# Kernel tuning notes

Measured on AMD Instinct MI355X. Metric: run time of the kernel, lower is better.

The kernel has to match this reference:

```python
import jax, jax.numpy as jnp
import numpy as np

N_USERS = 50000
N_ENTITIES = 100000
N_FACTORS = 8
N_RELATIONS = 17  # weight has n_relations-1 = 16 rows
EMB = 64
N_EDGES = 2_000_000
NNZ = 2_000_000
SLOPE = 0.2


def setup_inputs() -> dict:
    key = jax.random.key(0)
    ks = jax.random.split(key, 16)
    inp = {
        "entity_emb": jax.random.normal(ks[0], (N_ENTITIES, EMB), jnp.float32),
        "user_emb": jax.random.normal(ks[1], (N_USERS, EMB), jnp.float32),
        "latent_emb": jax.random.normal(ks[2], (N_FACTORS, EMB), jnp.float32),
        "edge_index": jax.random.randint(ks[3], (2, N_EDGES), 0, N_ENTITIES, jnp.int32),
        "edge_type": jax.random.randint(ks[4], (N_EDGES,), 1, N_RELATIONS, jnp.int32),
        "interact_rows": jax.random.randint(ks[5], (NNZ,), 0, N_USERS, jnp.int32),
        "interact_cols": jax.random.randint(ks[6], (NNZ,), 0, N_ENTITIES, jnp.int32),
        "interact_vals": jax.random.uniform(ks[7], (NNZ,), jnp.float32),
        "weight": jax.random.normal(ks[8], (N_RELATIONS - 1, EMB), jnp.float32),
        "entity_cate_set": jax.random.randint(ks[9], (N_ENTITIES,), 1, 33, jnp.int32),
        # params (torch Linear convention: y = x @ W.T + b)
        "W_user_att": jax.random.normal(ks[10], (N_FACTORS, N_FACTORS), jnp.float32) * 0.1,
        "b_user_att": jnp.zeros((N_FACTORS,), jnp.float32),
        "W_weight_att": jax.random.normal(ks[11], (N_RELATIONS - 1, N_RELATIONS - 1), jnp.float32) * 0.1,
        "b_weight_att": jnp.zeros((N_RELATIONS - 1,), jnp.float32),
        "W1": jax.random.normal(ks[12], (EMB, EMB), jnp.float32) * 0.1,
        "b1": jnp.zeros((EMB,), jnp.float32),
        "W2": jax.random.normal(ks[13], (EMB, EMB), jnp.float32) * 0.1,
        "b2": jnp.zeros((EMB,), jnp.float32),
    }
    return inp


def _lin(x, W, b):
    return x @ W.T + b


def reference(entity_emb, user_emb, latent_emb, edge_index, edge_type,
              interact_rows, interact_cols, interact_vals, weight, entity_cate_set,
              W_user_att, b_user_att, W_weight_att, b_weight_att, W1, b1, W2, b2):
    head, tail = edge_index[0], edge_index[1]

    # KG aggregate: gather-multiply-scatter_mean (is_div=False branch)
    neigh = entity_emb[tail] * weight[edge_type - 1]            # [E, C]
    sums = jax.ops.segment_sum(neigh, head, num_segments=N_ENTITIES)
    cnt = jax.ops.segment_sum(jnp.ones((neigh.shape[0],), neigh.dtype),
                              head, num_segments=N_ENTITIES)
    entity_agg = sums / jnp.maximum(cnt, 1.0)[:, None]          # [N_ent, C]

    # user aggregate: sparse mm (COO) interact_mat @ entity_emb
    user_agg = jax.ops.segment_sum(interact_vals[:, None] * entity_emb[interact_cols],
                                   interact_rows, num_segments=N_USERS)  # [U, C]

    # user -> latent interest attention
    score_ = _lin(user_emb, W1, b1) @ _lin(latent_emb, W1, b1).T          # [U, F]
    score = jax.nn.softmax(jax.nn.leaky_relu(_lin(score_, W_user_att, b_user_att), SLOPE), axis=1)  # [U, F]

    score_rp = _lin(latent_emb, W2, b2) @ _lin(weight, W2, b2).T          # [F, R-1]
    latent_new = jax.nn.softmax(jax.nn.leaky_relu(_lin(score_rp, W_weight_att, b_weight_att), SLOPE), axis=-1) @ weight  # [F, C]

    # (disen_weight * score).sum(dim=1) == score @ latent_new
    user_agg = user_agg * (score @ latent_new) + user_agg
    return (entity_agg, user_agg, latent_new)
```

## Files before the change

### kernel.cpp

```cpp
#include <hip/hip_runtime.h>

#define N_USERS    50000
#define N_ENTITIES 100000
#define EMB        64
#define N_EDGES    2000000
#define NNZ        2000000
#define SLOPE      0.2f

#define KROWS   256
#define KSHIFT  8
#define NBK     391
#define UROWS   128
#define USHIFT  7
#define NBU     391
#define CAPK    8192
#define CAPU    7680
#define CHUNK   8192
#define EPT     (CHUNK / 512)
#define PB      ((N_EDGES + CHUNK - 1) / CHUNK)
#define NQ      (NBK + NBU)
#define ACCBLK  512

__global__ __launch_bounds__(512) void hist_both(const int* __restrict__ head,
                                                 const int* __restrict__ urows,
                                                 int* __restrict__ kgOffs,
                                                 int* __restrict__ uOffs) {
    __shared__ int lhk[NBK];
    __shared__ int lhu[NBU];
    int tid = threadIdx.x;
    for (int t = tid; t < NBK; t += 512) lhk[t] = 0;
    for (int t = tid; t < NBU; t += 512) lhu[t] = 0;
    __syncthreads();
    int base = blockIdx.x * CHUNK;
#pragma unroll 4
    for (int j = 0; j < EPT; ++j) {
        int i = base + j * 512 + tid;
        if (i < N_EDGES) atomicAdd(&lhk[head[i] >> KSHIFT], 1);
        if (i < NNZ)     atomicAdd(&lhu[urows[i] >> USHIFT], 1);
    }
    __syncthreads();
    for (int t = tid; t < NBK; t += 512) { int c = lhk[t]; if (c) atomicAdd(&kgOffs[t], c); }
    for (int t = tid; t < NBU; t += 512) { int c = lhu[t]; if (c) atomicAdd(&uOffs[t], c); }
}

__global__ __launch_bounds__(512) void scan_both(int* __restrict__ kgOffs,
                                                 int* __restrict__ kgCur,
                                                 int* __restrict__ uOffs,
                                                 int* __restrict__ uCur) {
    __shared__ int tsum[512];
    int n     = (blockIdx.x == 0) ? NBK : NBU;
    int* offs = (blockIdx.x == 0) ? kgOffs : uOffs;
    int* cur  = (blockIdx.x == 0) ? kgCur  : uCur;
    int tid = threadIdx.x;
    int v = (tid < n) ? offs[tid] : 0;
    tsum[tid] = v;
    __syncthreads();
    for (int off = 1; off < 512; off <<= 1) {
        int t = (tid >= off) ? tsum[tid - off] : 0;
        __syncthreads();
        tsum[tid] += t;
        __syncthreads();
    }
    if (tid < n) { int e = tsum[tid] - v; offs[tid] = e; cur[tid] = e; }
    if (tid == n - 1) offs[n] = tsum[tid];
}

__device__ void small_dense_body(int l,
                                 const float* __restrict__ latent_emb,
                                 const float* __restrict__ weight,
                                 const float* __restrict__ W_weight_att,
                                 const float* __restrict__ b_weight_att,
                                 const float* __restrict__ W1,
                                 const float* __restrict__ b1,
                                 const float* __restrict__ W2,
                                 const float* __restrict__ b2,
                                 float* __restrict__ P_out,
                                 float* __restrict__ c_out,
                                 float* __restrict__ latent_new_out) {
    __shared__ float lat1[8 * 64];
    __shared__ float lat2[8 * 64];
    __shared__ float wl2[16 * 64];
    __shared__ float srp[8 * 16];
    __shared__ float soft[8 * 16];

    if (l < 64) {
        for (int f = 0; f < 8; ++f) {
            float a1 = b1[l], a2 = b2[l];
            for (int k = 0; k < 64; ++k) {
                float le = latent_emb[f * 64 + k];
                a1 += le * W1[l * 64 + k];
                a2 += le * W2[l * 64 + k];
            }
            lat1[f * 64 + l] = a1;
            lat2[f * 64 + l] = a2;
        }
        for (int r = 0; r < 16; ++r) {
            float a = b2[l];
            for (int k = 0; k < 64; ++k) a += weight[r * 64 + k] * W2[l * 64 + k];
            wl2[r * 64 + l] = a;
        }
    }
    __syncthreads();

    if (l < 64) {
        for (int f = 0; f < 8; ++f) {
            float p = 0.f;
            for (int d = 0; d < 64; ++d) p += W1[d * 64 + l] * lat1[f * 64 + d];
            P_out[l * 8 + f] = p;
        }
        if (l < 8) {
            float cc = 0.f;
            for (int d = 0; d < 64; ++d) cc += b1[d] * lat1[l * 64 + d];
            c_out[l] = cc;
        }
        for (int idx = l; idx < 128; idx += 64) {
            int f = idx >> 4, r = idx & 15;
            float a = 0.f;
            for (int d = 0; d < 64; ++d) a += lat2[f * 64 + d] * wl2[r * 64 + d];
            srp[idx] = a;
        }
    }
    __syncthreads();

    if (l < 8) {
        int f = l;
        float att[16];
        float mx = -1e30f;
        for (int k = 0; k < 16; ++k) {
            float a = b_weight_att[k];
            for (int j = 0; j < 16; ++j) a += srp[f * 16 + j] * W_weight_att[k * 16 + j];
            a = a > 0.f ? a : SLOPE * a;
            att[k] = a;
            mx = fmaxf(mx, a);
        }
        float s = 0.f;
        for (int k = 0; k < 16; ++k) { att[k] = expf(att[k] - mx); s += att[k]; }
        float inv = 1.f / s;
        for (int k = 0; k < 16; ++k) soft[f * 16 + k] = att[k] * inv;
    }
    __syncthreads();

    if (l < 64) {
        for (int f = 0; f < 8; ++f) {
            float a = 0.f;
            for (int r = 0; r < 16; ++r) a += soft[f * 16 + r] * weight[r * 64 + l];
            latent_new_out[f * 64 + l] = a;
        }
    }
}

__global__ void small_dense(const float* __restrict__ latent_emb,
                            const float* __restrict__ weight,
                            const float* __restrict__ W_weight_att,
                            const float* __restrict__ b_weight_att,
                            const float* __restrict__ W1,
                            const float* __restrict__ b1,
                            const float* __restrict__ W2,
                            const float* __restrict__ b2,
                            float* __restrict__ P_out,
                            float* __restrict__ c_out,
                            float* __restrict__ latent_new_out) {
    small_dense_body(threadIdx.x, latent_emb, weight, W_weight_att, b_weight_att,
                     W1, b1, W2, b2, P_out, c_out, latent_new_out);
}

__global__ __launch_bounds__(512) void scatter_both(const int* __restrict__ head,
                                                    const int* __restrict__ tail,
                                                    const int* __restrict__ etype,
                                                    int* __restrict__ kgCur,
                                                    int* __restrict__ kgPay,
                                                    const int* __restrict__ urows,
                                                    const int* __restrict__ ucols,
                                                    const float* __restrict__ uvals,
                                                    int* __restrict__ uCur,
                                                    int2* __restrict__ uPay,
                                                    const float* __restrict__ latent_emb,
                                                    const float* __restrict__ weight,
                                                    const float* __restrict__ W_weight_att,
                                                    const float* __restrict__ b_weight_att,
                                                    const float* __restrict__ W1,
                                                    const float* __restrict__ b1,
                                                    const float* __restrict__ W2,
                                                    const float* __restrict__ b2,
                                                    float* __restrict__ Pbuf,
                                                    float* __restrict__ cbuf,
                                                    float* __restrict__ lat_out) {
    if (blockIdx.x == 2 * PB) {
        small_dense_body(threadIdx.x, latent_emb, weight, W_weight_att,
                         b_weight_att, W1, b1, W2, b2, Pbuf, cbuf, lat_out);
        return;
    }

    __shared__ int lh[NBK];
    __shared__ int lb[NBK];
    int tid = threadIdx.x;
    bool isKg = blockIdx.x < PB;
    int base = (isKg ? blockIdx.x : blockIdx.x - PB) * CHUNK;
    int nTot = isKg ? N_EDGES : NNZ;
    int shift = isKg ? KSHIFT : USHIFT;
    const int* src = isKg ? head : urows;
    int* cur = isKg ? kgCur : uCur;

    for (int t = tid; t < NBK; t += 512) lh[t] = 0;
    __syncthreads();

    int hreg[EPT];
#pragma unroll
    for (int j = 0; j < EPT; ++j) {
        int i = base + j * 512 + tid;
        int h = (i < nTot) ? src[i] : -1;
        hreg[j] = h;
        if (h >= 0) atomicAdd(&lh[h >> shift], 1);
    }
    __syncthreads();
    for (int t = tid; t < NBK; t += 512) {
        int c = lh[t];
        lb[t] = c ? atomicAdd(&cur[t], c) : 0;
        lh[t] = 0;
    }
    __syncthreads();
    if (isKg) {
#pragma unroll
        for (int j = 0; j < EPT; ++j) {
            int h = hreg[j];
            if (h >= 0) {
                int i = base + j * 512 + tid;
                int b = h >> KSHIFT;
                int p = lb[b] + atomicAdd(&lh[b], 1);
                kgPay[p] = tail[i] | ((etype[i] - 1) << 17) | ((h & (KROWS - 1)) << 21);
            }
        }
    } else {
#pragma unroll
        for (int j = 0; j < EPT; ++j) {
            int h = hreg[j];
            if (h >= 0) {
                int i = base + j * 512 + tid;
                int b = h >> USHIFT;
                int p = lb[b] + atomicAdd(&lh[b], 1);
                uPay[p] = make_int2(ucols[i] | ((h & (UROWS - 1)) << 17),
                                    __float_as_int(uvals[i]));
            }
        }
    }
}

__global__ __launch_bounds__(1024, 8) void acc_both(
        const int* __restrict__ kgPay, const int* __restrict__ kgOffs,
        const int2* __restrict__ uPay, const int* __restrict__ uOffs,
        const float* __restrict__ entity_emb,
        const float* __restrict__ weight,
        const float* __restrict__ user_emb,
        const float* __restrict__ P,
        const float* __restrict__ cvec,
        const float* __restrict__ W_user_att,
        const float* __restrict__ b_user_att,
        const float* __restrict__ latent_new,
        int* __restrict__ qCtr,
        float* __restrict__ ent_out,
        float* __restrict__ user_out) {
    __shared__ long long smem8[7873];
    __shared__ int sbk;
    int t = threadIdx.x, d = t & 63, wv = t >> 6;

    for (;;) {
        __syncthreads();
        if (t == 0) sbk = atomicAdd(qCtr, 1);
        __syncthreads();
        int q = sbk;
        if (q >= NQ) return;

        if (q < NBU) {
            int2* spay = (int2*)smem8;
            int* lcnt = (int*)(spay + CAPU);
            int* lofs = lcnt + UROWS;
            int* sc   = lofs + UROWS + 1;
            int bk = q;
            int start = uOffs[bk], end = uOffs[bk + 1];
            int n = end - start; if (n > CAPU) n = CAPU;

            if (t < UROWS) lcnt[t] = 0;
            __syncthreads();
            for (int i = t; i < n; i += 1024)
                atomicAdd(&lcnt[(uPay[start + i].x >> 17) & (UROWS - 1)], 1);
            __syncthreads();
            if (t < UROWS) sc[t] = lcnt[t];
            __syncthreads();
            for (int off = 1; off < UROWS; off <<= 1) {
                int v = (t < UROWS && t >= off) ? sc[t - off] : 0;
                __syncthreads();
                if (t < UROWS) sc[t] += v;
                __syncthreads();
            }
            if (t < UROWS) { int e = sc[t] - lcnt[t]; lofs[t] = e; lcnt[t] = e; }
            if (t == 0) lofs[UROWS] = n;
            __syncthreads();
            for (int i = t; i < n; i += 1024) {
                int2 v = uPay[start + i];
                int p = atomicAdd(&lcnt[(v.x >> 17) & (UROWS - 1)], 1);
                spay[p] = v;
            }
            __syncthreads();

            int rowbase = bk * UROWS;
            for (int rr = 0; rr < UROWS / 16; ++rr) {
                int r = wv * (UROWS / 16) + rr;
                int gr = rowbase + r;
                if (gr >= N_USERS) break;
                int s0 = lofs[r], e0 = lofs[r + 1];
                float acc = 0.f;
                int i = s0;
                for (; i + 7 < e0; i += 8) {
                    float a0 = 0.f, a1 = 0.f;
#pragma unroll
                    for (int u = 0; u < 8; u += 2) {
                        int2 va = spay[i + u], vb = spay[i + u + 1];
                        a0 += __int_as_float(va.y) * entity_emb[(va.x & 0x1FFFF) * EMB + d];
                        a1 += __int_as_float(vb.y) * entity_emb[(vb.x & 0x1FFFF) * EMB + d];
                    }
                    acc += a0 + a1;
                }
                for (; i < e0; ++i) {
                    int2 v = spay[i];
                    acc += __int_as_float(v.y) * entity_emb[(v.x & 0x1FFFF) * EMB + d];
                }
                for (int j = start + CAPU; j < end; ++j) {
                    int2 v = uPay[j];
                    if (((v.x >> 17) & (UROWS - 1)) == r)
                        acc += __int_as_float(v.y) * entity_emb[(v.x & 0x1FFFF) * EMB + d];
                }

                float ue = user_emb[gr * EMB + d];
                float s[8];
#pragma unroll
                for (int f = 0; f < 8; ++f) s[f] = ue * P[d * 8 + f];
#pragma unroll
                for (int off = 32; off; off >>= 1) {
#pragma unroll
                    for (int f = 0; f < 8; ++f) s[f] += __shfl_xor(s[f], off, 64);
                }
#pragma unroll
                for (int f = 0; f < 8; ++f) s[f] += cvec[f];
                float att[8];
                float mx = -1e30f;
#pragma unroll
                for (int k = 0; k < 8; ++k) {
                    float a = b_user_att[k];
#pragma unroll
                    for (int j = 0; j < 8; ++j) a += s[j] * W_user_att[k * 8 + j];
                    a = a > 0.f ? a : SLOPE * a;
                    att[k] = a;
                    mx = fmaxf(mx, a);
                }
                float sum = 0.f;
#pragma unroll
                for (int k = 0; k < 8; ++k) { att[k] = __expf(att[k] - mx); sum += att[k]; }
                float inv = 1.f / sum;
                float g = 0.f;
#pragma unroll
                for (int f = 0; f < 8; ++f) g += att[f] * inv * latent_new[f * EMB + d];
                user_out[gr * EMB + d] = acc * (1.f + g);
            }
        } else {
            int* spay = (int*)smem8;
            int* lcnt = spay + CAPK;
            int* lofs = lcnt + KROWS;
            int* sc   = lofs + KROWS + 1;
            int bk = q - NBU;
            int start = kgOffs[bk], end = kgOffs[bk + 1];
            int n = end - start; if (n > CAPK) n = CAPK;

            if (t < KROWS) lcnt[t] = 0;
            __syncthreads();
            for (int i = t; i < n; i += 1024)
                atomicAdd(&lcnt[(kgPay[start + i] >> 21) & (KROWS - 1)], 1);
            __syncthreads();
            if (t < KROWS) sc[t] = lcnt[t];
            __syncthreads();
            for (int off = 1; off < KROWS; off <<= 1) {
                int v = (t < KROWS && t >= off) ? sc[t - off] : 0;
                __syncthreads();
                if (t < KROWS) sc[t] += v;
                __syncthreads();
            }
            if (t < KROWS) { int e = sc[t] - lcnt[t]; lofs[t] = e; lcnt[t] = e; }
            if (t == 0) lofs[KROWS] = n;
            __syncthreads();
            for (int i = t; i < n; i += 1024) {
                int v = kgPay[start + i];
                int p = atomicAdd(&lcnt[(v >> 21) & (KROWS - 1)], 1);
                spay[p] = v;
            }
            __syncthreads();

            int rowbase = bk * KROWS;
            for (int rr = 0; rr < KROWS / 16; ++rr) {
                int r = wv * (KROWS / 16) + rr;
                int gr = rowbase + r;
                if (gr >= N_ENTITIES) break;
                int s0 = lofs[r], e0 = lofs[r + 1];
                int cnt = e0 - s0;
                float acc = 0.f;
                int i = s0;
                for (; i + 7 < e0; i += 8) {
                    float a0 = 0.f, a1 = 0.f;
#pragma unroll
                    for (int u = 0; u < 8; u += 2) {
                        int va = spay[i + u], vb = spay[i + u + 1];
                        a0 += entity_emb[(va & 0x1FFFF) * EMB + d] * weight[((va >> 17) & 15) * EMB + d];
                        a1 += entity_emb[(vb & 0x1FFFF) * EMB + d] * weight[((vb >> 17) & 15) * EMB + d];
                    }
                    acc += a0 + a1;
                }
                for (; i < e0; ++i) {
                    int v = spay[i];
                    acc += entity_emb[(v & 0x1FFFF) * EMB + d] * weight[((v >> 17) & 15) * EMB + d];
                }
                for (int j = start + CAPK; j < end; ++j) {
                    int v = kgPay[j];
                    if (((v >> 21) & (KROWS - 1)) == r) {
                        acc += entity_emb[(v & 0x1FFFF) * EMB + d] * weight[((v >> 17) & 15) * EMB + d];
                        ++cnt;
                    }
                }
                ent_out[gr * EMB + d] = acc / fmaxf((float)cnt, 1.f);
            }
        }
    }
}

__global__ void kg_scatter(const int* __restrict__ head, const int* __restrict__ tail,
                           const int* __restrict__ etype,
                           const float* __restrict__ entity_emb,
                           const float* __restrict__ weight,
                           float* __restrict__ sums, float* __restrict__ cnt) {
    int gid = blockIdx.x * blockDim.x + threadIdx.x;
    int e = gid >> 6, d = threadIdx.x & 63;
    if (e >= N_EDGES) return;
    int h = head[e], t = tail[e], w = etype[e] - 1;
    float v = entity_emb[t * EMB + d] * weight[w * EMB + d];
    unsafeAtomicAdd(&sums[h * EMB + d], v);
    if (d == 0) unsafeAtomicAdd(&cnt[h], 1.0f);
}

__global__ void user_scatter(const int* __restrict__ rows, const int* __restrict__ cols,
                             const float* __restrict__ vals,
                             const float* __restrict__ entity_emb,
                             float* __restrict__ user_sums) {
    int gid = blockIdx.x * blockDim.x + threadIdx.x;
    int e = gid >> 6, d = threadIdx.x & 63;
    if (e >= NNZ) return;
    float v = vals[e] * entity_emb[cols[e] * EMB + d];
    unsafeAtomicAdd(&user_sums[rows[e] * EMB + d], v);
}

__global__ void entity_div(float* __restrict__ ent, const float* __restrict__ cnt) {
    int gid = blockIdx.x * blockDim.x + threadIdx.x;
    if (gid >= N_ENTITIES * EMB) return;
    float c = cnt[gid >> 6];
    ent[gid] = ent[gid] / fmaxf(c, 1.0f);
}

__global__ void user_finalize(const float* __restrict__ user_emb,
                              const float* __restrict__ P,
                              const float* __restrict__ c,
                              const float* __restrict__ W_user_att,
                              const float* __restrict__ b_user_att,
                              const float* __restrict__ latent_new,
                              float* __restrict__ user_out) {
    int gid = blockIdx.x * blockDim.x + threadIdx.x;
    int u = gid >> 6, lane = threadIdx.x & 63;
    if (u >= N_USERS) return;
    float ue = user_emb[u * 64 + lane];
    float s[8];
#pragma unroll
    for (int f = 0; f < 8; ++f) s[f] = ue * P[lane * 8 + f];
#pragma unroll
    for (int off = 32; off; off >>= 1)
#pragma unroll
        for (int f = 0; f < 8; ++f) s[f] += __shfl_xor(s[f], off, 64);
#pragma unroll
    for (int f = 0; f < 8; ++f) s[f] += c[f];
    float att[8], mx = -1e30f;
#pragma unroll
    for (int k = 0; k < 8; ++k) {
        float a = b_user_att[k];
#pragma unroll
        for (int j = 0; j < 8; ++j) a += s[j] * W_user_att[k * 8 + j];
        a = a > 0.f ? a : SLOPE * a;
        att[k] = a;
        mx = fmaxf(mx, a);
    }
    float sum = 0.f;
#pragma unroll
    for (int k = 0; k < 8; ++k) { att[k] = expf(att[k] - mx); sum += att[k]; }
    float inv = 1.f / sum, g = 0.f;
#pragma unroll
    for (int f = 0; f < 8; ++f) g += att[f] * inv * latent_new[f * 64 + lane];
    float ua = user_out[u * 64 + lane];
    user_out[u * 64 + lane] = ua * (1.f + g);
}

extern "C" void kernel_launch(void* const* d_in, const int* in_sizes, int n_in,
                              void* d_out, int out_size, void* d_ws, size_t ws_size,
                              hipStream_t stream) {
    const float* entity_emb   = (const float*)d_in[0];
    const float* user_emb     = (const float*)d_in[1];
    const float* latent_emb   = (const float*)d_in[2];
    const int*   edge_index   = (const int*)d_in[3];
    const int*   edge_type    = (const int*)d_in[4];
    const int*   irows        = (const int*)d_in[5];
    const int*   icols        = (const int*)d_in[6];
    const float* ivals        = (const float*)d_in[7];
    const float* weight       = (const float*)d_in[8];
    const float* W_user_att   = (const float*)d_in[10];
    const float* b_user_att   = (const float*)d_in[11];
    const float* W_weight_att = (const float*)d_in[12];
    const float* b_weight_att = (const float*)d_in[13];
    const float* W1           = (const float*)d_in[14];
    const float* b1           = (const float*)d_in[15];
    const float* W2           = (const float*)d_in[16];
    const float* b2           = (const float*)d_in[17];

    float* out      = (float*)d_out;
    float* ent_out  = out;
    float* user_out = out + (size_t)N_ENTITIES * EMB;
    float* lat_out  = user_out + (size_t)N_USERS * EMB;

    const int* head = edge_index;
    const int* tail = edge_index + N_EDGES;

    int* ws_i = (int*)d_ws;
    int*   kgOffs = ws_i;
    int*   uOffs  = kgOffs + (NBK + 1);
    int*   qCtr   = uOffs + (NBU + 1);
    int*   kgCur  = qCtr + 2;
    int*   uCur   = kgCur + NBK;
    int*   kgPay  = uCur + NBU;
    int2*  uPay   = (int2*)(kgPay + N_EDGES);
    float* Pbuf   = (float*)(uPay + NNZ);
    float* cbuf   = Pbuf + 64 * 8;
    size_t need_bytes = (size_t)((NBK + 1) + (NBU + 1) + 2 + NBK + NBU +
                                 N_EDGES + 2 * (size_t)NNZ + 512 + 8) * 4;

    if (ws_size >= need_bytes) {
        hipMemsetAsync(kgOffs, 0,
                       (size_t)((NBK + 1) + (NBU + 1) + 2) * sizeof(int), stream);

        hist_both<<<PB, 512, 0, stream>>>(head, irows, kgOffs, uOffs);
        scan_both<<<2, 512, 0, stream>>>(kgOffs, kgCur, uOffs, uCur);
        scatter_both<<<2 * PB + 1, 512, 0, stream>>>(head, tail, edge_type, kgCur, kgPay,
                                                     irows, icols, ivals, uCur, uPay,
                                                     latent_emb, weight, W_weight_att,
                                                     b_weight_att, W1, b1, W2, b2,
                                                     Pbuf, cbuf, lat_out);
        acc_both<<<ACCBLK, 1024, 0, stream>>>(kgPay, kgOffs, uPay, uOffs,
                                              entity_emb, weight, user_emb,
                                              Pbuf, cbuf, W_user_att, b_user_att,
                                              lat_out, qCtr, ent_out, user_out);
    } else {
        float* cnt   = (float*)d_ws;
        float* Pbuf2 = cnt + N_ENTITIES;
        float* cbuf2 = Pbuf2 + 64 * 8;
        hipMemsetAsync(ent_out, 0,
                       (size_t)(N_ENTITIES + N_USERS) * EMB * sizeof(float), stream);
        hipMemsetAsync(cnt, 0, N_ENTITIES * sizeof(float), stream);
        int blocks_edges = (N_EDGES * 64) / 256;
        kg_scatter<<<blocks_edges, 256, 0, stream>>>(head, tail, edge_type, entity_emb,
                                                     weight, ent_out, cnt);
        user_scatter<<<blocks_edges, 256, 0, stream>>>(irows, icols, ivals, entity_emb,
                                                       user_out);
        small_dense<<<1, 64, 0, stream>>>(latent_emb, weight, W_weight_att,
                                          b_weight_att, W1, b1, W2, b2,
                                          Pbuf2, cbuf2, lat_out);
        user_finalize<<<(N_USERS * 64) / 256, 256, 0, stream>>>(user_emb, Pbuf2, cbuf2,
                                                                W_user_att, b_user_att,
                                                                lat_out, user_out);
        entity_div<<<(N_ENTITIES * EMB) / 256, 256, 0, stream>>>(ent_out, cnt);
    }
}
```

Before: 397.7 us.

## Replace barrier-heavy local scans with wavefront shuffle scan and register-cached payloads

In the accumulate kernel, each bucket's payload is now loaded once into registers and reused for both the local count pass and the scatter into shared memory, instead of being read from global memory twice. The per-bucket prefix scan over row counts, which took many block-wide barrier steps, becomes a single-wavefront shuffle scan. The histogram kernel becomes a grid-stride launch of 1024 blocks of 256 threads, and CHUNK is halved, which doubles the scatter kernel's grid. Holding 8 payload entries per thread adds register pressure to a kernel launched with 1024 threads.

Result: slower. 453.6 us (+14.1%).

```diff
diff --git a/kernel.cpp b/kernel.cpp
--- a/kernel.cpp
+++ b/kernel.cpp
@@ -15,32 +15,30 @@
 #define NBU     391
 #define CAPK    8192
 #define CAPU    7680
-#define CHUNK   8192
+#define CHUNK   4096
 #define EPT     (CHUNK / 512)
 #define PB      ((N_EDGES + CHUNK - 1) / CHUNK)
+#define HB      1024
 #define NQ      (NBK + NBU)
 #define ACCBLK  512
 
-__global__ __launch_bounds__(512) void hist_both(const int* __restrict__ head,
+__global__ __launch_bounds__(256) void hist_both(const int* __restrict__ head,
                                                  const int* __restrict__ urows,
                                                  int* __restrict__ kgOffs,
                                                  int* __restrict__ uOffs) {
     __shared__ int lhk[NBK];
     __shared__ int lhu[NBU];
     int tid = threadIdx.x;
-    for (int t = tid; t < NBK; t += 512) lhk[t] = 0;
-    for (int t = tid; t < NBU; t += 512) lhu[t] = 0;
-    __syncthreads();
-    int base = blockIdx.x * CHUNK;
-#pragma unroll 4
-    for (int j = 0; j < EPT; ++j) {
-        int i = base + j * 512 + tid;
-        if (i < N_EDGES) atomicAdd(&lhk[head[i] >> KSHIFT], 1);
-        if (i < NNZ)     atomicAdd(&lhu[urows[i] >> USHIFT], 1);
-    }
-    __syncthreads();
-    for (int t = tid; t < NBK; t += 512) { int c = lhk[t]; if (c) atomicAdd(&kgOffs[t], c); }
-    for (int t = tid; t < NBU; t += 512) { int c = lhu[t]; if (c) atomicAdd(&uOffs[t], c); }
+    for (int t = tid; t < NBK; t += 256) lhk[t] = 0;
+    for (int t = tid; t < NBU; t += 256) lhu[t] = 0;
+    __syncthreads();
+    for (int i = blockIdx.x * 256 + tid; i < N_EDGES; i += HB * 256) {
+        atomicAdd(&lhk[head[i]  >> KSHIFT], 1);
+        atomicAdd(&lhu[urows[i] >> USHIFT], 1);
+    }
+    __syncthreads();
+    for (int t = tid; t < NBK; t += 256) { int c = lhk[t]; if (c) atomicAdd(&kgOffs[t], c); }
+    for (int t = tid; t < NBU; t += 256) { int c = lhu[t]; if (c) atomicAdd(&uOffs[t], c); }
 }
 
 __global__ __launch_bounds__(512) void scan_both(int* __restrict__ kgOffs,
@@ -262,6 +260,7 @@
     __shared__ long long smem8[7873];
     __shared__ int sbk;
     int t = threadIdx.x, d = t & 63, wv = t >> 6;
+    int lane = d;
 
     for (;;) {
         __syncthreads();
@@ -274,31 +273,43 @@
             int2* spay = (int2*)smem8;
             int* lcnt = (int*)(spay + CAPU);
             int* lofs = lcnt + UROWS;
-            int* sc   = lofs + UROWS + 1;
             int bk = q;
             int start = uOffs[bk], end = uOffs[bk + 1];
             int n = end - start; if (n > CAPU) n = CAPU;
 
             if (t < UROWS) lcnt[t] = 0;
             __syncthreads();
-            for (int i = t; i < n; i += 1024)
-                atomicAdd(&lcnt[(uPay[start + i].x >> 17) & (UROWS - 1)], 1);
-            __syncthreads();
-            if (t < UROWS) sc[t] = lcnt[t];
-            __syncthreads();
-            for (int off = 1; off < UROWS; off <<= 1) {
-                int v = (t < UROWS && t >= off) ? sc[t - off] : 0;
-                __syncthreads();
-                if (t < UROWS) sc[t] += v;
-                __syncthreads();
-            }
-            if (t < UROWS) { int e = sc[t] - lcnt[t]; lofs[t] = e; lcnt[t] = e; }
-            if (t == 0) lofs[UROWS] = n;
-            __syncthreads();
-            for (int i = t; i < n; i += 1024) {
-                int2 v = uPay[start + i];
-                int p = atomicAdd(&lcnt[(v.x >> 17) & (UROWS - 1)], 1);
-                spay[p] = v;
+            int2 rv[8];
+#pragma unroll
+            for (int j = 0; j < 8; ++j) {
+                int i = t + j * 1024;
+                if (i < n) {
+                    rv[j] = uPay[start + i];
+                    atomicAdd(&lcnt[(rv[j].x >> 17) & (UROWS - 1)], 1);
+                }
+            }
+            __syncthreads();
+            if (wv == 0) {
+                int c0 = lcnt[2 * lane], c1 = lcnt[2 * lane + 1];
+                int s = c0 + c1, incl = s;
+#pragma unroll
+                for (int off = 1; off < 64; off <<= 1) {
+                    int o = __shfl_up(incl, off, 64);
+                    if (lane >= off) incl += o;
+                }
+                int excl = incl - s;
+                lofs[2 * lane] = excl;       lcnt[2 * lane] = excl;
+                lofs[2 * lane + 1] = excl + c0; lcnt[2 * lane + 1] = excl + c0;
+                if (lane == 63) lofs[UROWS] = incl;
+            }
+            __syncthreads();
+#pragma unroll
+            for (int j = 0; j < 8; ++j) {
+                int i = t + j * 1024;
+                if (i < n) {
+                    int p = atomicAdd(&lcnt[(rv[j].x >> 17) & (UROWS - 1)], 1);
+                    spay[p] = rv[j];
+                }
             }
             __syncthreads();
 
@@ -365,31 +376,47 @@
             int* spay = (int*)smem8;
             int* lcnt = spay + CAPK;
             int* lofs = lcnt + KROWS;
-            int* sc   = lofs + KROWS + 1;
             int bk = q - NBU;
             int start = kgOffs[bk], end = kgOffs[bk + 1];
             int n = end - start; if (n > CAPK) n = CAPK;
 
             if (t < KROWS) lcnt[t] = 0;
             __syncthreads();
-            for (int i = t; i < n; i += 1024)
-                atomicAdd(&lcnt[(kgPay[start + i] >> 21) & (KROWS - 1)], 1);
-            __syncthreads();
-            if (t < KROWS) sc[t] = lcnt[t];
-            __syncthreads();
-            for (int off = 1; off < KROWS; off <<= 1) {
-                int v = (t < KROWS && t >= off) ? sc[t - off] : 0;
-                __syncthreads();
-                if (t < KROWS) sc[t] += v;
-                __syncthreads();
-            }
-            if (t < KROWS) { int e = sc[t] - lcnt[t]; lofs[t] = e; lcnt[t] = e; }
-            if (t == 0) lofs[KROWS] = n;
-            __syncthreads();
-            for (int i = t; i < n; i += 1024) {
-                int v = kgPay[start + i];
-                int p = atomicAdd(&lcnt[(v >> 21) & (KROWS - 1)], 1);
-                spay[p] = v;
+            int rvk[8];
+#pragma unroll
+            for (int j = 0; j < 8; ++j) {
+                int i = t + j * 1024;
+                if (i < n) {
+                    rvk[j] = kgPay[start + i];
+                    atomicAdd(&lcnt[(rvk[j] >> 21) & (KROWS - 1)], 1);
+                }
+            }
+            __syncthreads();
+            if (wv == 0) {
+                int c0 = lcnt[4 * lane], c1 = lcnt[4 * lane + 1];
+                int c2 = lcnt[4 * lane + 2], c3 = lcnt[4 * lane + 3];
+                int s = c0 + c1 + c2 + c3, incl = s;
+#pragma unroll
+                for (int off = 1; off < 64; off <<= 1) {
+                    int o = __shfl_up(incl, off, 64);
+                    if (lane >= off) incl += o;
+                }
+                int excl = incl - s;
+                lofs[4 * lane] = excl;                 lcnt[4 * lane] = excl;
+                lofs[4 * lane + 1] = excl + c0;        lcnt[4 * lane + 1] = excl + c0;
+                lofs[4 * lane + 2] = excl + c0 + c1;   lcnt[4 * lane + 2] = excl + c0 + c1;
+                lofs[4 * lane + 3] = excl + c0 + c1 + c2;
+                lcnt[4 * lane + 3] = excl + c0 + c1 + c2;
+                if (lane == 63) lofs[KROWS] = incl;
+            }
+            __syncthreads();
+#pragma unroll
+            for (int j = 0; j < 8; ++j) {
+                int i = t + j * 1024;
+                if (i < n) {
+                    int p = atomicAdd(&lcnt[(rvk[j] >> 21) & (KROWS - 1)], 1);
+                    spay[p] = rvk[j];
+                }
             }
             __syncthreads();
 
@@ -547,7 +574,7 @@
         hipMemsetAsync(kgOffs, 0,
                        (size_t)((NBK + 1) + (NBU + 1) + 2) * sizeof(int), stream);
 
-        hist_both<<<PB, 512, 0, stream>>>(head, irows, kgOffs, uOffs);
+        hist_both<<<HB, 256, 0, stream>>>(head, irows, kgOffs, uOffs);
         scan_both<<<2, 512, 0, stream>>>(kgOffs, kgCur, uOffs, uCur);
         scatter_both<<<2 * PB + 1, 512, 0, stream>>>(head, tail, edge_type, kgCur, kgPay,
                                                      irows, icols, ivals, uCur, uPay,
```

## Fuse histogram, scan and scatter into one cooperative kernel; wavefront-shuffle local scans

Applied to the files above, without the earlier changes.

Replaces the three partition kernels (hist, scan, scatter) with one cooperative-launch kernel that uses grid syncs, keeps head/row indices in registers between the histogram and scatter phases so they are read only once, and does the small dense computation in the last block. Inside acc_both, the shared-memory Hillis-Steele scans over row counts become a single-wavefront shuffle scan, which removes many block barriers. Risks: grid.sync cost, occupancy limits on the cooperative launch (512 blocks × 512 threads), and a fallback path taken if the cooperative launch fails.

Measured after the change: 568.0 us. 42.8% more time.

```diff
diff --git a/kernel.cpp b/kernel.cpp
--- a/kernel.cpp
+++ b/kernel.cpp
@@ -1,4 +1,7 @@
 #include <hip/hip_runtime.h>
+#include <hip/hip_cooperative_groups.h>
+
+namespace cg = cooperative_groups;
 
 #define N_USERS    50000
 #define N_ENTITIES 100000
@@ -21,49 +24,9 @@
 #define NQ      (NBK + NBU)
 #define ACCBLK  512
 
-__global__ __launch_bounds__(512) void hist_both(const int* __restrict__ head,
-                                                 const int* __restrict__ urows,
-                                                 int* __restrict__ kgOffs,
-                                                 int* __restrict__ uOffs) {
-    __shared__ int lhk[NBK];
-    __shared__ int lhu[NBU];
-    int tid = threadIdx.x;
-    for (int t = tid; t < NBK; t += 512) lhk[t] = 0;
-    for (int t = tid; t < NBU; t += 512) lhu[t] = 0;
-    __syncthreads();
-    int base = blockIdx.x * CHUNK;
-#pragma unroll 4
-    for (int j = 0; j < EPT; ++j) {
-        int i = base + j * 512 + tid;
-        if (i < N_EDGES) atomicAdd(&lhk[head[i] >> KSHIFT], 1);
-        if (i < NNZ)     atomicAdd(&lhu[urows[i] >> USHIFT], 1);
-    }
-    __syncthreads();
-    for (int t = tid; t < NBK; t += 512) { int c = lhk[t]; if (c) atomicAdd(&kgOffs[t], c); }
-    for (int t = tid; t < NBU; t += 512) { int c = lhu[t]; if (c) atomicAdd(&uOffs[t], c); }
-}
-
-__global__ __launch_bounds__(512) void scan_both(int* __restrict__ kgOffs,
-                                                 int* __restrict__ kgCur,
-                                                 int* __restrict__ uOffs,
-                                                 int* __restrict__ uCur) {
-    __shared__ int tsum[512];
-    int n     = (blockIdx.x == 0) ? NBK : NBU;
-    int* offs = (blockIdx.x == 0) ? kgOffs : uOffs;
-    int* cur  = (blockIdx.x == 0) ? kgCur  : uCur;
-    int tid = threadIdx.x;
-    int v = (tid < n) ? offs[tid] : 0;
-    tsum[tid] = v;
-    __syncthreads();
-    for (int off = 1; off < 512; off <<= 1) {
-        int t = (tid >= off) ? tsum[tid - off] : 0;
-        __syncthreads();
-        tsum[tid] += t;
-        __syncthreads();
-    }
-    if (tid < n) { int e = tsum[tid] - v; offs[tid] = e; cur[tid] = e; }
-    if (tid == n - 1) offs[n] = tsum[tid];
-}
+#define FBLK    512
+#define KCH     ((N_EDGES + FBLK - 1) / FBLK)
+#define FEPT    ((KCH + 511) / 512)
 
 __device__ void small_dense_body(int l,
                                  const float* __restrict__ latent_emb,
@@ -162,6 +125,164 @@
                             float* __restrict__ latent_new_out) {
     small_dense_body(threadIdx.x, latent_emb, weight, W_weight_att, b_weight_att,
                      W1, b1, W2, b2, P_out, c_out, latent_new_out);
+}
+
+__global__ __launch_bounds__(512, 4) void part_fused(
+        const int* __restrict__ head,
+        const int* __restrict__ tail,
+        const int* __restrict__ etype,
+        int* __restrict__ kgOffs,
+        int* __restrict__ kgCur,
+        int* __restrict__ kgPay,
+        const int* __restrict__ urows,
+        const int* __restrict__ ucols,
+        const float* __restrict__ uvals,
+        int* __restrict__ uOffs,
+        int* __restrict__ uCur,
+        int2* __restrict__ uPay,
+        const float* __restrict__ latent_emb,
+        const float* __restrict__ weight,
+        const float* __restrict__ W_weight_att,
+        const float* __restrict__ b_weight_att,
+        const float* __restrict__ W1,
+        const float* __restrict__ b1,
+        const float* __restrict__ W2,
+        const float* __restrict__ b2,
+        float* __restrict__ Pbuf,
+        float* __restrict__ cbuf,
+        float* __restrict__ lat_out) {
+    cg::grid_group grid = cg::this_grid();
+    __shared__ int lhk[NBK];
+    __shared__ int lhu[NBU];
+    __shared__ int lbk[NBK];
+    __shared__ int lbu[NBU];
+    __shared__ int tsum[512];
+    int tid = threadIdx.x, b = blockIdx.x;
+
+    for (int t = tid; t < NBK; t += 512) { lhk[t] = 0; lhu[t] = 0; }
+    __syncthreads();
+
+    int base = b * KCH;
+    int bend = base + KCH; if (bend > N_EDGES) bend = N_EDGES;
+
+    int hk[FEPT], hu[FEPT];
+#pragma unroll
+    for (int j = 0; j < FEPT; ++j) {
+        int i = base + j * 512 + tid;
+        int h = (i < bend) ? head[i]  : -1;
+        int r = (i < bend) ? urows[i] : -1;
+        hk[j] = h; hu[j] = r;
+        if (h >= 0) atomicAdd(&lhk[h >> KSHIFT], 1);
+        if (r >= 0) atomicAdd(&lhu[r >> USHIFT], 1);
+    }
+    __syncthreads();
+    for (int t = tid; t < NBK; t += 512) { int c = lhk[t]; if (c) atomicAdd(&kgOffs[t], c); }
+    for (int t = tid; t < NBU; t += 512) { int c = lhu[t]; if (c) atomicAdd(&uOffs[t], c); }
+
+    grid.sync();
+
+    if (b < 2) {
+        int n     = (b == 0) ? NBK : NBU;
+        int* offs = (b == 0) ? kgOffs : uOffs;
+        int* cur  = (b == 0) ? kgCur  : uCur;
+        int v = (tid < n) ? offs[tid] : 0;
+        tsum[tid] = v;
+        __syncthreads();
+        for (int off = 1; off < 512; off <<= 1) {
+            int t = (tid >= off) ? tsum[tid - off] : 0;
+            __syncthreads();
+            tsum[tid] += t;
+            __syncthreads();
+        }
+        if (tid < n) { int e = tsum[tid] - v; offs[tid] = e; cur[tid] = e; }
+        if (tid == n - 1) offs[n] = tsum[tid];
+    }
+
+    grid.sync();
+
+    for (int t = tid; t < NBK; t += 512) {
+        int c = lhk[t];
+        lbk[t] = c ? atomicAdd(&kgCur[t], c) : 0;
+        lhk[t] = 0;
+    }
+    for (int t = tid; t < NBU; t += 512) {
+        int c = lhu[t];
+        lbu[t] = c ? atomicAdd(&uCur[t], c) : 0;
+        lhu[t] = 0;
+    }
+    __syncthreads();
+
+#pragma unroll
+    for (int j = 0; j < FEPT; ++j) {
+        int h = hk[j];
+        if (h >= 0) {
+            int i = base + j * 512 + tid;
+            int bkt = h >> KSHIFT;
+            int p = lbk[bkt] + atomicAdd(&lhk[bkt], 1);
+            kgPay[p] = tail[i] | ((etype[i] - 1) << 17) | ((h & (KROWS - 1)) << 21);
+        }
+    }
+#pragma unroll
+    for (int j = 0; j < FEPT; ++j) {
+        int r = hu[j];
+        if (r >= 0) {
+            int i = base + j * 512 + tid;
+            int bkt = r >> USHIFT;
+            int p = lbu[bkt] + atomicAdd(&lhu[bkt], 1);
+            uPay[p] = make_int2(ucols[i] | ((r & (UROWS - 1)) << 17),
+                                __float_as_int(uvals[i]));
+        }
+    }
+
+    if (b == FBLK - 1) {
+        __syncthreads();
+        small_dense_body(tid, latent_emb, weight, W_weight_att, b_weight_att,
+                         W1, b1, W2, b2, Pbuf, cbuf, lat_out);
+    }
+}
+
+__global__ __launch_bounds__(512) void hist_both(const int* __restrict__ head,
+                                                 const int* __restrict__ urows,
+                                                 int* __restrict__ kgOffs,
+                                                 int* __restrict__ uOffs) {
+    __shared__ int lhk[NBK];
+    __shared__ int lhu[NBU];
+    int tid = threadIdx.x;
+    for (int t = tid; t < NBK; t += 512) lhk[t] = 0;
+    for (int t = tid; t < NBU; t += 512) lhu[t] = 0;
+    __syncthreads();
+    int base = blockIdx.x * CHUNK;
+#pragma unroll 4
+    for (int j = 0; j < EPT; ++j) {
+        int i = base + j * 512 + tid;
+        if (i < N_EDGES) atomicAdd(&lhk[head[i] >> KSHIFT], 1);
+        if (i < NNZ)     atomicAdd(&lhu[urows[i] >> USHIFT], 1);
+    }
+    __syncthreads();
+    for (int t = tid; t < NBK; t += 512) { int c = lhk[t]; if (c) atomicAdd(&kgOffs[t], c); }
+    for (int t = tid; t < NBU; t += 512) { int c = lhu[t]; if (c) atomicAdd(&uOffs[t], c); }
+}
+
+__global__ __launch_bounds__(512) void scan_both(int* __restrict__ kgOffs,
+                                                 int* __restrict__ kgCur,
+                                                 int* __restrict__ uOffs,
+                                                 int* __restrict__ uCur) {
+    __shared__ int tsum[512];
+    int n     = (blockIdx.x == 0) ? NBK : NBU;
+    int* offs = (blockIdx.x == 0) ? kgOffs : uOffs;
+    int* cur  = (blockIdx.x == 0) ? kgCur  : uCur;
+    int tid = threadIdx.x;
+    int v = (tid < n) ? offs[tid] : 0;
+    tsum[tid] = v;
+    __syncthreads();
+    for (int off = 1; off < 512; off <<= 1) {
+        int t = (tid >= off) ? tsum[tid - off] : 0;
+        __syncthreads();
+        tsum[tid] += t;
+        __syncthreads();
+    }
+    if (tid < n) { int e = tsum[tid] - v; offs[tid] = e; cur[tid] = e; }
+    if (tid == n - 1) offs[n] = tsum[tid];
 }
 
 __global__ __launch_bounds__(512) void scatter_both(const int* __restrict__ head,
@@ -262,6 +383,7 @@
     __shared__ long long smem8[7873];
     __shared__ int sbk;
     int t = threadIdx.x, d = t & 63, wv = t >> 6;
+    int lane = d;
 
     for (;;) {
         __syncthreads();
@@ -274,7 +396,6 @@
             int2* spay = (int2*)smem8;
             int* lcnt = (int*)(spay + CAPU);
             int* lofs = lcnt + UROWS;
-            int* sc   = lofs + UROWS + 1;
             int bk = q;
             int start = uOffs[bk], end = uOffs[bk + 1];
             int n = end - start; if (n > CAPU) n = CAPU;
@@ -284,16 +405,19 @@
             for (int i = t; i < n; i += 1024)
                 atomicAdd(&lcnt[(uPay[start + i].x >> 17) & (UROWS - 1)], 1);
             __syncthreads();
-            if (t < UROWS) sc[t] = lcnt[t];
-            __syncthreads();
-            for (int off = 1; off < UROWS; off <<= 1) {
-                int v = (t < UROWS && t >= off) ? sc[t - off] : 0;
-                __syncthreads();
-                if (t < UROWS) sc[t] += v;
-                __syncthreads();
-            }
-            if (t < UROWS) { int e = sc[t] - lcnt[t]; lofs[t] = e; lcnt[t] = e; }
-            if (t == 0) lofs[UROWS] = n;
+            if (wv == 0) {
+                int c0 = lcnt[2 * lane], c1 = lcnt[2 * lane + 1];
+                int s = c0 + c1, incl = s;
+#pragma unroll
+                for (int off = 1; off < 64; off <<= 1) {
+                    int o = __shfl_up(incl, off, 64);
+                    if (lane >= off) incl += o;
+                }
+                int excl = incl - s;
+                lofs[2 * lane] = excl;          lcnt[2 * lane] = excl;
+                lofs[2 * lane + 1] = excl + c0; lcnt[2 * lane + 1] = excl + c0;
+                if (lane == 63) lofs[UROWS] = incl;
+            }
             __syncthreads();
             for (int i = t; i < n; i += 1024) {
                 int2 v = uPay[start + i];
@@ -365,7 +489,6 @@
             int* spay = (int*)smem8;
             int* lcnt = spay + CAPK;
             int* lofs = lcnt + KROWS;
-            int* sc   = lofs + KROWS + 1;
             int bk = q - NBU;
             int start = kgOffs[bk], end = kgOffs[bk + 1];
             int n = end - start; if (n > CAPK) n = CAPK;
@@ -375,16 +498,22 @@
             for (int i = t; i < n; i += 1024)
                 atomicAdd(&lcnt[(kgPay[start + i] >> 21) & (KROWS - 1)], 1);
             __syncthreads();
-            if (t < KROWS) sc[t] = lcnt[t];
-            __syncthreads();
-            for (int off = 1; off < KROWS; off <<= 1) {
-                int v = (t < KROWS && t >= off) ? sc[t - off] : 0;
-                __syncthreads();
-                if (t < KROWS) sc[t] += v;
-                __syncthreads();
-            }
-            if (t < KROWS) { int e = sc[t] - lcnt[t]; lofs[t] = e; lcnt[t] = e; }
-            if (t == 0) lofs[KROWS] = n;
+            if (wv == 0) {
+                int c0 = lcnt[4 * lane], c1 = lcnt[4 * lane + 1];
+                int c2 = lcnt[4 * lane + 2], c3 = lcnt[4 * lane + 3];
+                int s = c0 + c1 + c2 + c3, incl = s;
+#pragma unroll
+                for (int off = 1; off < 64; off <<= 1) {
+                    int o = __shfl_up(incl, off, 64);
+                    if (lane >= off) incl += o;
+                }
+                int excl = incl - s;
+                lofs[4 * lane] = excl;                    lcnt[4 * lane] = excl;
+                lofs[4 * lane + 1] = excl + c0;           lcnt[4 * lane + 1] = excl + c0;
+                lofs[4 * lane + 2] = excl + c0 + c1;      lcnt[4 * lane + 2] = excl + c0 + c1;
+                lofs[4 * lane + 3] = excl + c0 + c1 + c2; lcnt[4 * lane + 3] = excl + c0 + c1 + c2;
+                if (lane == 63) lofs[KROWS] = incl;
+            }
             __syncthreads();
             for (int i = t; i < n; i += 1024) {
                 int v = kgPay[start + i];
@@ -547,13 +676,31 @@
         hipMemsetAsync(kgOffs, 0,
                        (size_t)((NBK + 1) + (NBU + 1) + 2) * sizeof(int), stream);
 
-        hist_both<<<PB, 512, 0, stream>>>(head, irows, kgOffs, uOffs);
-        scan_both<<<2, 512, 0, stream>>>(kgOffs, kgCur, uOffs, uCur);
-        scatter_both<<<2 * PB + 1, 512, 0, stream>>>(head, tail, edge_type, kgCur, kgPay,
-                                                     irows, icols, ivals, uCur, uPay,
-                                                     latent_emb, weight, W_weight_att,
-                                                     b_weight_att, W1, b1, W2, b2,
-                                                     Pbuf, cbuf, lat_out);
+        void* cargs[] = {
+            (void*)&head, (void*)&tail, (void*)&edge_type,
+            (void*)&kgOffs, (void*)&kgCur, (void*)&kgPay,
+            (void*)&irows, (void*)&icols, (void*)&ivals,
+            (void*)&uOffs, (void*)&uCur, (void*)&uPay,
+            (void*)&latent_emb, (void*)&weight,
+            (void*)&W_weight_att, (void*)&b_weight_att,
+            (void*)&W1, (void*)&b1, (void*)&W2, (void*)&b2,
+            (void*)&Pbuf, (void*)&cbuf, (void*)&lat_out
+        };
+        hipError_t ce = hipLaunchCooperativeKernel((const void*)part_fused,
+                                                   dim3(FBLK), dim3(512),
+                                                   cargs, 0, stream);
+        if (ce != hipSuccess) {
+            hist_both<<<PB, 512, 0, stream>>>(head, irows, kgOffs, uOffs);
+            scan_both<<<2, 512, 0, stream>>>(kgOffs, kgCur, uOffs, uCur);
+            scatter_both<<<2 * PB + 1, 512, 0, stream>>>(head, tail, edge_type,
+                                                         kgCur, kgPay,
+                                                         irows, icols, ivals,
+                                                         uCur, uPay,
+                                                         latent_emb, weight,
+                                                         W_weight_att, b_weight_att,
+                                                         W1, b1, W2, b2,
+                                                         Pbuf, cbuf, lat_out);
+        }
         acc_both<<<ACCBLK, 1024, 0, stream>>>(kgPay, kgOffs, uPay, uOffs,
                                               entity_emb, weight, user_emb,
                                               Pbuf, cbuf, W_user_att, b_user_att,
```

## Stage bucketed payloads in shared memory for coalesced scatter writes

Applied to the files above, without the earlier changes.

The scatter kernel now sorts each chunk's payloads locally in LDS using a block-wide prefix scan over bucket counts, then writes them out contiguously per bucket. A binary search over the local offsets maps each slot to its global position. This turns random per-element global writes into mostly coalesced runs. The user chunk size is halved so its int2 payloads fit in the shared buffer. The cost is extra syncs, a scan and a binary search per element, plus a larger LDS footprint (about 40 KB) that may reduce occupancy.

Result: no change. 398.2 us (+0.1%).

```diff
diff --git a/kernel.cpp b/kernel.cpp
--- a/kernel.cpp
+++ b/kernel.cpp
@@ -15,9 +15,13 @@
 #define NBU     391
 #define CAPK    8192
 #define CAPU    7680
-#define CHUNK   8192
-#define EPT     (CHUNK / 512)
-#define PB      ((N_EDGES + CHUNK - 1) / CHUNK)
+#define HCH     8192
+#define HEPT    (HCH / 512)
+#define HPB     ((N_EDGES + HCH - 1) / HCH)
+#define CHK_K   8192
+#define PB_K    ((N_EDGES + CHK_K - 1) / CHK_K)
+#define CHK_U   4096
+#define PB_U    ((NNZ + CHK_U - 1) / CHK_U)
 #define NQ      (NBK + NBU)
 #define ACCBLK  512
 
@@ -31,9 +35,9 @@
     for (int t = tid; t < NBK; t += 512) lhk[t] = 0;
     for (int t = tid; t < NBU; t += 512) lhu[t] = 0;
     __syncthreads();
-    int base = blockIdx.x * CHUNK;
+    int base = blockIdx.x * HCH;
 #pragma unroll 4
-    for (int j = 0; j < EPT; ++j) {
+    for (int j = 0; j < HEPT; ++j) {
         int i = base + j * 512 + tid;
         if (i < N_EDGES) atomicAdd(&lhk[head[i] >> KSHIFT], 1);
         if (i < NNZ)     atomicAdd(&lhu[urows[i] >> USHIFT], 1);
@@ -185,62 +189,115 @@
                                                     float* __restrict__ Pbuf,
                                                     float* __restrict__ cbuf,
                                                     float* __restrict__ lat_out) {
-    if (blockIdx.x == 2 * PB) {
+    if (blockIdx.x == PB_K + PB_U) {
         small_dense_body(threadIdx.x, latent_emb, weight, W_weight_att,
                          b_weight_att, W1, b1, W2, b2, Pbuf, cbuf, lat_out);
         return;
     }
 
+    __shared__ long long sp8[4096];
     __shared__ int lh[NBK];
     __shared__ int lb[NBK];
+    __shared__ int lofs[NBK + 1];
+    __shared__ int sc[512];
     int tid = threadIdx.x;
-    bool isKg = blockIdx.x < PB;
-    int base = (isKg ? blockIdx.x : blockIdx.x - PB) * CHUNK;
-    int nTot = isKg ? N_EDGES : NNZ;
-    int shift = isKg ? KSHIFT : USHIFT;
-    const int* src = isKg ? head : urows;
-    int* cur = isKg ? kgCur : uCur;
+    bool isKg = blockIdx.x < PB_K;
 
     for (int t = tid; t < NBK; t += 512) lh[t] = 0;
     __syncthreads();
 
-    int hreg[EPT];
-#pragma unroll
-    for (int j = 0; j < EPT; ++j) {
-        int i = base + j * 512 + tid;
-        int h = (i < nTot) ? src[i] : -1;
-        hreg[j] = h;
-        if (h >= 0) atomicAdd(&lh[h >> shift], 1);
-    }
-    __syncthreads();
-    for (int t = tid; t < NBK; t += 512) {
-        int c = lh[t];
-        lb[t] = c ? atomicAdd(&cur[t], c) : 0;
-        lh[t] = 0;
-    }
-    __syncthreads();
     if (isKg) {
-#pragma unroll
-        for (int j = 0; j < EPT; ++j) {
-            int h = hreg[j];
+        int base = blockIdx.x * CHK_K;
+        int n = N_EDGES - base; if (n > CHK_K) n = CHK_K;
+        int* spk = (int*)sp8;
+
+        int kreg[CHK_K / 512];
+#pragma unroll
+        for (int j = 0; j < CHK_K / 512; ++j) {
+            int o = j * 512 + tid;
+            int h = (o < n) ? head[base + o] : -1;
+            kreg[j] = h;
+            if (h >= 0) atomicAdd(&lh[h >> KSHIFT], 1);
+        }
+        __syncthreads();
+        for (int t = tid; t < NBK; t += 512)
+            lb[t] = lh[t] ? atomicAdd(&kgCur[t], lh[t]) : 0;
+        int v = (tid < NBK) ? lh[tid] : 0;
+        sc[tid] = v;
+        __syncthreads();
+        for (int off = 1; off < 512; off <<= 1) {
+            int t = (tid >= off) ? sc[tid - off] : 0;
+            __syncthreads();
+            sc[tid] += t;
+            __syncthreads();
+        }
+        if (tid < NBK) { int e = sc[tid] - v; lofs[tid] = e; lh[tid] = e; }
+        if (tid == NBK - 1) lofs[NBK] = sc[tid];
+        __syncthreads();
+#pragma unroll
+        for (int j = 0; j < CHK_K / 512; ++j) {
+            int h = kreg[j];
             if (h >= 0) {
                 int i = base + j * 512 + tid;
-                int b = h >> KSHIFT;
-                int p = lb[b] + atomicAdd(&lh[b], 1);
-                kgPay[p] = tail[i] | ((etype[i] - 1) << 17) | ((h & (KROWS - 1)) << 21);
-            }
+                int p = atomicAdd(&lh[h >> KSHIFT], 1);
+                spk[p] = tail[i] | ((etype[i] - 1) << 17) | ((h & (KROWS - 1)) << 21);
+            }
+        }
+        __syncthreads();
+        for (int i = tid; i < n; i += 512) {
+            int lo = 0, hi = NBK;
+            while (hi - lo > 1) {
+                int mid = (lo + hi) >> 1;
+                if (lofs[mid] <= i) lo = mid; else hi = mid;
+            }
+            kgPay[lb[lo] + (i - lofs[lo])] = spk[i];
         }
     } else {
-#pragma unroll
-        for (int j = 0; j < EPT; ++j) {
-            int h = hreg[j];
-            if (h >= 0) {
+        int base = (blockIdx.x - PB_K) * CHK_U;
+        int n = NNZ - base; if (n > CHK_U) n = CHK_U;
+        int2* spu = (int2*)sp8;
+
+        int kreg[CHK_U / 512];
+#pragma unroll
+        for (int j = 0; j < CHK_U / 512; ++j) {
+            int o = j * 512 + tid;
+            int r = (o < n) ? urows[base + o] : -1;
+            kreg[j] = r;
+            if (r >= 0) atomicAdd(&lh[r >> USHIFT], 1);
+        }
+        __syncthreads();
+        for (int t = tid; t < NBU; t += 512)
+            lb[t] = lh[t] ? atomicAdd(&uCur[t], lh[t]) : 0;
+        int v = (tid < NBU) ? lh[tid] : 0;
+        sc[tid] = v;
+        __syncthreads();
+        for (int off = 1; off < 512; off <<= 1) {
+            int t = (tid >= off) ? sc[tid - off] : 0;
+            __syncthreads();
+            sc[tid] += t;
+            __syncthreads();
+        }
+        if (tid < NBU) { int e = sc[tid] - v; lofs[tid] = e; lh[tid] = e; }
+        if (tid == NBU - 1) lofs[NBU] = sc[tid];
+        __syncthreads();
+#pragma unroll
+        for (int j = 0; j < CHK_U / 512; ++j) {
+            int r = kreg[j];
+            if (r >= 0) {
                 int i = base + j * 512 + tid;
-                int b = h >> USHIFT;
-                int p = lb[b] + atomicAdd(&lh[b], 1);
-                uPay[p] = make_int2(ucols[i] | ((h & (UROWS - 1)) << 17),
-                                    __float_as_int(uvals[i]));
-            }
+                int p = atomicAdd(&lh[r >> USHIFT], 1);
+                spu[p] = make_int2(ucols[i] | ((r & (UROWS - 1)) << 17),
+                                   __float_as_int(uvals[i]));
+            }
+        }
+        __syncthreads();
+        for (int i = tid; i < n; i += 512) {
+            int lo = 0, hi = NBU;
+            while (hi - lo > 1) {
+                int mid = (lo + hi) >> 1;
+                if (lofs[mid] <= i) lo = mid; else hi = mid;
+            }
+            uPay[lb[lo] + (i - lofs[lo])] = spu[i];
         }
     }
 }
@@ -547,13 +604,16 @@
         hipMemsetAsync(kgOffs, 0,
                        (size_t)((NBK + 1) + (NBU + 1) + 2) * sizeof(int), stream);
 
-        hist_both<<<PB, 512, 0, stream>>>(head, irows, kgOffs, uOffs);
+        hist_both<<<HPB, 512, 0, stream>>>(head, irows, kgOffs, uOffs);
         scan_both<<<2, 512, 0, stream>>>(kgOffs, kgCur, uOffs, uCur);
-        scatter_both<<<2 * PB + 1, 512, 0, stream>>>(head, tail, edge_type, kgCur, kgPay,
-                                                     irows, icols, ivals, uCur, uPay,
-                                                     latent_emb, weight, W_weight_att,
-                                                     b_weight_att, W1, b1, W2, b2,
-                                                     Pbuf, cbuf, lat_out);
+        scatter_both<<<PB_K + PB_U + 1, 512, 0, stream>>>(head, tail, edge_type,
+                                                          kgCur, kgPay,
+                                                          irows, icols, ivals,
+                                                          uCur, uPay,
+                                                          latent_emb, weight,
+                                                          W_weight_att, b_weight_att,
+                                                          W1, b1, W2, b2,
+                                                          Pbuf, cbuf, lat_out);
         acc_both<<<ACCBLK, 1024, 0, stream>>>(kgPay, kgOffs, uPay, uOffs,
                                               entity_emb, weight, user_emb,
                                               Pbuf, cbuf, W_user_att, b_user_att,
```
